# Kernel tuning notes

Hardware: AMD Instinct MI355X
Metric: run time of the kernel (lower is better)

The kernel has to match this reference:

```python
import jax, jax.numpy as jnp
import numpy as np

B, D, UD = 32, 1024, 256          # batch, chunks_dim, units_dim
ENT, NENT = 32, 64                # entity_size, n_entities
S, C = NENT * ENT, NENT + 1       # src_len (units), n_chunks
NEG_INF = float('-inf')


def setup_inputs() -> dict:
    key = jax.random.key(0)
    ks = jax.random.split(key, 9)
    source = jax.random.normal(ks[0], (B, D), jnp.float32)
    high_level_repr = jax.random.normal(ks[1], (C, B, D), jnp.float32)
    pos_embs = jax.random.normal(ks[2], (S, B, UD), jnp.float32)
    low_level_repr = jax.random.normal(ks[3], (S, B, D), jnp.float32)
    low_level_mask = jax.random.randint(ks[4], (NENT, B, ENT), 0, 2).astype(bool)
    high_level_mask = jax.random.randint(ks[5], (1, B, C), 0, 2).astype(bool)
    high_level_mask = high_level_mask.at[..., 0].set(False)  # avoid all-masked chunk softmax
    W_unit = jax.random.normal(ks[6], (UD, D), jnp.float32) / np.sqrt(D)
    W_chunk = jax.random.normal(ks[7], (D, D), jnp.float32) / np.sqrt(D)
    W_out = jax.random.normal(ks[8], (D, 2 * D), jnp.float32) / np.sqrt(2 * D)
    return {"source": source, "high_level_repr": high_level_repr, "pos_embs": pos_embs,
            "low_level_repr": low_level_repr, "low_level_mask": low_level_mask,
            "high_level_mask": high_level_mask, "W_unit": W_unit, "W_chunk": W_chunk,
            "W_out": W_out}


def reference(source, high_level_repr, pos_embs, low_level_repr,
              low_level_mask, high_level_mask, W_unit, W_chunk, W_out):
    # batch-first views (torch transposes(0,1))
    hl = jnp.swapaxes(high_level_repr, 0, 1)    # (B, C, D)
    ll = jnp.swapaxes(low_level_repr, 0, 1)     # (B, S, D)
    pe = jnp.swapaxes(pos_embs, 0, 1)           # (B, S, UD)
    ll_mask = jnp.swapaxes(low_level_mask, 0, 1)   # (B, NENT, ENT)
    hl_mask = jnp.swapaxes(high_level_mask, 0, 1)  # (B, 1, C)

    # 'general' attention scorers, tgt_len == 1
    q_u = source @ W_unit.T                      # (B, UD)
    align_units = jnp.einsum('bd,bsd->bs', q_u, pe)        # (B, S)
    q_c = source @ W_chunk.T                     # (B, D)
    align_chunks = jnp.einsum('bd,bcd->bc', q_c, hl)[:, None, :]  # (B, 1, C)

    # low-level masked softmax per entity, NaN rows -> 0
    au = align_units.reshape(B, NENT, ENT)
    au = jnp.where(ll_mask, NEG_INF, au)
    au = jax.nn.softmax(au, axis=-1)
    all_masked = jnp.all(ll_mask, axis=-1)       # (B, NENT) rows that were NaN
    au = jnp.where(all_masked[..., None], 0.0, au)
    au = au.reshape(B, 1, S)

    # high-level masked softmax, drop chunk 0, inflate to unit granularity
    ac = jnp.where(hl_mask, NEG_INF, align_chunks)
    ac = jax.nn.softmax(ac, axis=-1)[:, :, 1:]   # (B, 1, C-1)
    ac_inflated = jnp.repeat(ac, ENT, axis=-1)   # (B, 1, S)

    align_vectors = ac_inflated * au             # (B, 1, S)
    c = jnp.einsum('bts,bsd->btd', align_vectors, ll)  # (B, 1, D)
    concat = jnp.concatenate([c, source[:, None, :]], axis=-1).reshape(B, 2 * D)
    attn_h = jnp.tanh(concat @ W_out.T)          # (B, D); tanh since attn_type='general'

    return (attn_h,
            align_vectors[:, 0, :],              # (B, S)
            ac[:, 0, :],                         # (B, C-1)
            au.reshape(B, S))                    # (B, S)
```

## Files before the change

### kernel.cpp

```cpp
#include <hip/hip_runtime.h>

#define B 32
#define D 1024
#define UD 256
#define ENT 32
#define NENT 64
#define S 2048
#define C 65
#define NSLAB 8
#define SROWS 256

__device__ __forceinline__ float dot4(float4 w, const float* q) {
    return w.x * q[0] + w.y * q[1] + w.z * q[2] + w.w * q[3];
}

__global__ __launch_bounds__(256) void k_proj(const float* __restrict__ src,
                                              const float* __restrict__ Wu,
                                              const float* __restrict__ Wc,
                                              float* __restrict__ qu,
                                              float* __restrict__ qc) {
    __shared__ alignas(16) float s_src[4][D];
    __shared__ float red[4][64][4];
    int t = threadIdx.x, rg = blockIdx.x, bg = blockIdx.y;
    for (int f = t; f < 4 * (D / 4); f += 256) {
        int bb = f >> 8, i4 = f & 255;
        float4 v = *(const float4*)(src + (size_t)(bg * 4 + bb) * D + i4 * 4);
        *(float4*)(&s_src[bb][i4 * 4]) = v;
    }
    __syncthreads();
    int jl = t & 63, kq = t >> 6;
    int gj = rg * 64 + jl;
    const float* wrow = (gj < UD) ? (Wu + (size_t)gj * D) : (Wc + (size_t)(gj - UD) * D);
    const float4* wp = (const float4*)wrow + kq * 64;
    float acc[4] = {0.f, 0.f, 0.f, 0.f};
#pragma unroll 4
    for (int i = 0; i < 64; ++i) {
        float4 w = wp[i];
        int k = kq * 256 + i * 4;
#pragma unroll
        for (int bb = 0; bb < 4; ++bb) acc[bb] += dot4(w, &s_src[bb][k]);
    }
#pragma unroll
    for (int bb = 0; bb < 4; ++bb) red[kq][jl][bb] = acc[bb];
    __syncthreads();
    {
        int jl2 = t & 63, bb = t >> 6;
        float s = red[0][jl2][bb] + red[1][jl2][bb] + red[2][jl2][bb] + red[3][jl2][bb];
        int gj2 = rg * 64 + jl2, b = bg * 4 + bb;
        if (gj2 < UD) qu[b * UD + gj2] = s;
        else qc[b * D + (gj2 - UD)] = s;
    }
}

__global__ __launch_bounds__(256) void k_score(const float* __restrict__ hl,
                                               const float* __restrict__ qc,
                                               float* __restrict__ sc) {
    __shared__ float red[4];
    int c = blockIdx.x, b = blockIdx.y, t = threadIdx.x;
    const float4* hp = (const float4*)(hl + ((size_t)c * B + b) * D);
    const float4* qp = (const float4*)(qc + (size_t)b * D);
    float4 h = hp[t];
    float4 q = qp[t];
    float acc = h.x * q.x + h.y * q.y + h.z * q.z + h.w * q.w;
    for (int o = 32; o >= 1; o >>= 1) acc += __shfl_xor(acc, o);
    if ((t & 63) == 0) red[t >> 6] = acc;
    __syncthreads();
    if (t == 0) sc[b * C + c] = red[0] + red[1] + red[2] + red[3];
}

__global__ __launch_bounds__(512) void k_fused(const float* __restrict__ pe,
                                               const float* __restrict__ ll,
                                               const int* __restrict__ lmask,
                                               const int* __restrict__ hmask,
                                               const float* __restrict__ qu,
                                               const float* __restrict__ sc,
                                               float* __restrict__ pf,
                                               float* __restrict__ out_au,
                                               float* __restrict__ out_ac,
                                               float* __restrict__ out_av) {
    __shared__ alignas(16) float q[UD];
    __shared__ float s_ac[NENT];
    __shared__ float s_sc[SROWS];
    __shared__ float s_av[SROWS];
    __shared__ alignas(16) float4 s_red[256];
    int ss = blockIdx.x, b = blockIdx.y, t = threadIdx.x;

    if (t < UD) q[t] = qu[b * UD + t];

    if (t < 64) {
        bool m1 = hmask[b * C + t] != 0;
        float x1 = m1 ? -1e30f : sc[b * C + t];
        float x2 = -1e30f;
        bool m2 = true;
        if (t == 0) { m2 = hmask[b * C + 64] != 0; x2 = m2 ? -1e30f : sc[b * C + 64]; }
        float mx = fmaxf(x1, x2);
        for (int o = 32; o >= 1; o >>= 1) mx = fmaxf(mx, __shfl_xor(mx, o));
        float e1 = m1 ? 0.f : __expf(x1 - mx);
        float sm = e1 + ((t == 0 && !m2) ? __expf(x2 - mx) : 0.f);
        for (int o = 32; o >= 1; o >>= 1) sm += __shfl_xor(sm, o);
        bool mc = hmask[b * C + (t + 1)] != 0;
        float xc = mc ? 0.f : sc[b * C + (t + 1)];
        float p = mc ? 0.f : __expf(xc - mx) / sm;
        s_ac[t] = p;
        if (ss == 0) out_ac[b * NENT + t] = p;
    }
    __syncthreads();

    int rg = t >> 3, r = t & 7;
#pragma unroll
    for (int pass = 0; pass < 4; ++pass) {
        int j = pass * 64 + rg;
        int s = ss * SROWS + j;
        const float4* pp = (const float4*)(pe + ((size_t)s * B + b) * UD) + r;
        float acc = 0.f;
#pragma unroll
        for (int i = 0; i < 8; ++i) {
            float4 v = pp[i * 8];
            acc += dot4(v, &q[(r + i * 8) * 4]);
        }
        for (int o = 1; o < 8; o <<= 1) acc += __shfl_xor(acc, o);
        if (r == 0) s_sc[j] = acc;
    }
    __syncthreads();

    if (t < SROWS) {
        int j = t, e = j & 31;
        int n = ss * 8 + (j >> 5);
        bool m = lmask[((size_t)n * B + b) * ENT + e] != 0;
        float v = m ? -1e30f : s_sc[j];
        float mx = v;
        for (int o = 16; o >= 1; o >>= 1) mx = fmaxf(mx, __shfl_xor(mx, o));
        float p = m ? 0.f : __expf(v - mx);
        float sm = p;
        for (int o = 16; o >= 1; o >>= 1) sm += __shfl_xor(sm, o);
        float au = (sm > 0.f) ? p / sm : 0.f;
        float av = s_ac[n] * au;
        s_av[j] = av;
        int s = ss * SROWS + j;
        out_au[b * S + s] = au;
        out_av[b * S + s] = av;
    }
    __syncthreads();

    int half = t >> 8, tt = t & 255;
    float4 acc = {0.f, 0.f, 0.f, 0.f};
    const float4* base =
        (const float4*)(ll + ((size_t)(ss * SROWS + half * 128) * B + b) * D) + tt;
#pragma unroll 8
    for (int j = 0; j < 128; ++j) {
        float4 x = base[(size_t)j * (B * D / 4)];
        float w = s_av[half * 128 + j];
        acc.x += w * x.x;
        acc.y += w * x.y;
        acc.z += w * x.z;
        acc.w += w * x.w;
    }
    if (half == 1) s_red[tt] = acc;
    __syncthreads();
    if (half == 0) {
        float4 o = s_red[tt];
        acc.x += o.x; acc.y += o.y; acc.z += o.z; acc.w += o.w;
        *(float4*)(pf + ((size_t)ss * B + b) * D + tt * 4) = acc;
    }
}

__global__ __launch_bounds__(256) void k_out(const float* __restrict__ Wo,
                                             const float* __restrict__ src,
                                             const float* __restrict__ pf,
                                             float* __restrict__ out_h) {
    __shared__ alignas(16) float cc[4][2 * D];
    __shared__ float red[4][64][4];
    int t = threadIdx.x, jg = blockIdx.x, bg = blockIdx.y;
    for (int f = t; f < 4 * (2 * D / 4); f += 256) {
        int bb = f >> 9, part = f & 511;
        int b = bg * 4 + bb;
        float4 v;
        if (part < 256) {
            float4 a = {0.f, 0.f, 0.f, 0.f};
            const float4* pp = (const float4*)(pf + (size_t)b * D) + part;
#pragma unroll
            for (int ssi = 0; ssi < NSLAB; ++ssi) {
                float4 x = pp[(size_t)ssi * (B * D / 4)];
                a.x += x.x; a.y += x.y; a.z += x.z; a.w += x.w;
            }
            v = a;
        } else {
            v = *(const float4*)(src + (size_t)b * D + (part - 256) * 4);
        }
        *(float4*)(&cc[bb][part * 4]) = v;
    }
    __syncthreads();
    int jl = t & 63, kq = t >> 6;
    int j = jg * 64 + jl;
    const float4* wp = (const float4*)(Wo + (size_t)j * 2 * D) + kq * 128;
    float acc[4] = {0.f, 0.f, 0.f, 0.f};
#pragma unroll 4
    for (int i = 0; i < 128; ++i) {
        float4 w = wp[i];
        int k = kq * 512 + i * 4;
#pragma unroll
        for (int bb = 0; bb < 4; ++bb) acc[bb] += dot4(w, &cc[bb][k]);
    }
#pragma unroll
    for (int bb = 0; bb < 4; ++bb) red[kq][jl][bb] = acc[bb];
    __syncthreads();
    {
        int jl2 = t & 63, bb = t >> 6;
        float s = red[0][jl2][bb] + red[1][jl2][bb] + red[2][jl2][bb] + red[3][jl2][bb];
        out_h[(size_t)(bg * 4 + bb) * D + jg * 64 + jl2] = tanhf(s);
    }
}

extern "C" void kernel_launch(void* const* d_in, const int* in_sizes, int n_in,
                              void* d_out, int out_size, void* d_ws, size_t ws_size,
                              hipStream_t stream) {
    const float* src = (const float*)d_in[0];
    const float* hl = (const float*)d_in[1];
    const float* pe = (const float*)d_in[2];
    const float* ll = (const float*)d_in[3];
    const int* lmask = (const int*)d_in[4];
    const int* hmask = (const int*)d_in[5];
    const float* Wu = (const float*)d_in[6];
    const float* Wc = (const float*)d_in[7];
    const float* Wo = (const float*)d_in[8];

    float* out = (float*)d_out;
    float* out_h = out;
    float* out_av = out + B * D;
    float* out_ac = out_av + B * S;
    float* out_au = out_ac + B * NENT;

    float* ws = (float*)d_ws;
    float* qu = ws;
    float* qc = qu + B * UD;
    float* scb = qc + B * D;
    float* pf = scb + B * C;

    k_proj<<<dim3(20, 8), 256, 0, stream>>>(src, Wu, Wc, qu, qc);
    k_score<<<dim3(C, B), 256, 0, stream>>>(hl, qc, scb);
    k_fused<<<dim3(NSLAB, B), 512, 0, stream>>>(pe, ll, lmask, hmask, qu, scb,
                                                pf, out_au, out_ac, out_av);
    k_out<<<dim3(16, 8), 256, 0, stream>>>(Wo, src, pf, out_h);
}
```

Baseline: 461.8 us.

## Restructure fused attention kernel to one wavefront per entity, removing block barriers

Each 64-lane wavefront now owns one entity of 32 units. Within its wave it recomputes the chunk softmax, computes the unit scores with full-wave shuffle reductions, runs the per-entity softmax, and accumulates the weighted low-level rows with four float4 loads per lane. Partial sums are combined across the 8 waves through shared memory behind a single barrier, so the earlier staging of scores and weights in shared memory and its multiple __syncthreads are gone. The cost is redundant chunk-softmax work in every wave and more shuffle reductions per score row.

```diff
diff --git a/kernel.cpp b/kernel.cpp
--- a/kernel.cpp
+++ b/kernel.cpp
@@ -8,7 +8,6 @@
 #define S 2048
 #define C 65
 #define NSLAB 8
-#define SROWS 256
 
 __device__ __forceinline__ float dot4(float4 w, const float* q) {
     return w.x * q[0] + w.y * q[1] + w.z * q[2] + w.w * q[3];
@@ -78,89 +77,81 @@
                                                float* __restrict__ out_au,
                                                float* __restrict__ out_ac,
                                                float* __restrict__ out_av) {
-    __shared__ alignas(16) float q[UD];
-    __shared__ float s_ac[NENT];
-    __shared__ float s_sc[SROWS];
-    __shared__ float s_av[SROWS];
-    __shared__ alignas(16) float4 s_red[256];
+    __shared__ alignas(16) float4 s_part[NSLAB][256];
     int ss = blockIdx.x, b = blockIdx.y, t = threadIdx.x;
-
-    if (t < UD) q[t] = qu[b * UD + t];
-
-    if (t < 64) {
-        bool m1 = hmask[b * C + t] != 0;
-        float x1 = m1 ? -1e30f : sc[b * C + t];
-        float x2 = -1e30f;
-        bool m2 = true;
-        if (t == 0) { m2 = hmask[b * C + 64] != 0; x2 = m2 ? -1e30f : sc[b * C + 64]; }
-        float mx = fmaxf(x1, x2);
-        for (int o = 32; o >= 1; o >>= 1) mx = fmaxf(mx, __shfl_xor(mx, o));
-        float e1 = m1 ? 0.f : __expf(x1 - mx);
-        float sm = e1 + ((t == 0 && !m2) ? __expf(x2 - mx) : 0.f);
-        for (int o = 32; o >= 1; o >>= 1) sm += __shfl_xor(sm, o);
-        bool mc = hmask[b * C + (t + 1)] != 0;
-        float xc = mc ? 0.f : sc[b * C + (t + 1)];
-        float p = mc ? 0.f : __expf(xc - mx) / sm;
-        s_ac[t] = p;
-        if (ss == 0) out_ac[b * NENT + t] = p;
-    }
-    __syncthreads();
-
-    int rg = t >> 3, r = t & 7;
-#pragma unroll
-    for (int pass = 0; pass < 4; ++pass) {
-        int j = pass * 64 + rg;
-        int s = ss * SROWS + j;
-        const float4* pp = (const float4*)(pe + ((size_t)s * B + b) * UD) + r;
-        float acc = 0.f;
-#pragma unroll
-        for (int i = 0; i < 8; ++i) {
-            float4 v = pp[i * 8];
-            acc += dot4(v, &q[(r + i * 8) * 4]);
+    int w = t >> 6, l = t & 63;
+    int n = ss * NSLAB + w;
+
+    bool m1 = hmask[b * C + l] != 0;
+    float x1 = m1 ? -1e30f : sc[b * C + l];
+    bool m2 = hmask[b * C + 64] != 0;
+    float x2 = m2 ? -1e30f : sc[b * C + 64];
+    float mx = x1;
+    for (int o = 32; o >= 1; o >>= 1) mx = fmaxf(mx, __shfl_xor(mx, o));
+    mx = fmaxf(mx, x2);
+    float e1 = m1 ? 0.f : __expf(x1 - mx);
+    float sm = e1;
+    for (int o = 32; o >= 1; o >>= 1) sm += __shfl_xor(sm, o);
+    float e2 = m2 ? 0.f : __expf(x2 - mx);
+    sm += e2;
+    int c = n + 1;
+    float en = (c < 64) ? __shfl(e1, c) : e2;
+    float ac = en / sm;
+    if (l == 0) out_ac[b * NENT + n] = ac;
+
+    float4 qf = ((const float4*)(qu + (size_t)b * UD))[l];
+    int s0 = n * ENT;
+    const float4* pe4 = (const float4*)pe;
+    float score = 0.f;
+#pragma unroll 4
+    for (int j = 0; j < ENT; ++j) {
+        float4 v = pe4[((size_t)(s0 + j) * B + b) * (UD / 4) + l];
+        float p = v.x * qf.x + v.y * qf.y + v.z * qf.z + v.w * qf.w;
+        for (int o = 32; o >= 1; o >>= 1) p += __shfl_xor(p, o);
+        score = (l == j) ? p : score;
+    }
+
+    int e = l & 31;
+    bool m = lmask[((size_t)n * B + b) * ENT + e] != 0;
+    float v = m ? -1e30f : score;
+    float emx = v;
+    for (int o = 16; o >= 1; o >>= 1) emx = fmaxf(emx, __shfl_xor(emx, o));
+    float p = m ? 0.f : __expf(v - emx);
+    float esm = p;
+    for (int o = 16; o >= 1; o >>= 1) esm += __shfl_xor(esm, o);
+    float au = (esm > 0.f) ? p / esm : 0.f;
+    float av = ac * au;
+    if (l < ENT) {
+        out_au[b * S + s0 + l] = au;
+        out_av[b * S + s0 + l] = av;
+    }
+
+    float4 a0 = {0.f, 0.f, 0.f, 0.f}, a1 = a0, a2 = a0, a3 = a0;
+    const float4* ll4 = (const float4*)ll;
+#pragma unroll 4
+    for (int j = 0; j < ENT; ++j) {
+        float wv = __shfl(av, j);
+        const float4* rp = ll4 + ((size_t)(s0 + j) * B + b) * (D / 4) + l;
+        float4 x0 = rp[0], x1v = rp[64], x2v = rp[128], x3v = rp[192];
+        a0.x += wv * x0.x;  a0.y += wv * x0.y;  a0.z += wv * x0.z;  a0.w += wv * x0.w;
+        a1.x += wv * x1v.x; a1.y += wv * x1v.y; a1.z += wv * x1v.z; a1.w += wv * x1v.w;
+        a2.x += wv * x2v.x; a2.y += wv * x2v.y; a2.z += wv * x2v.z; a2.w += wv * x2v.w;
+        a3.x += wv * x3v.x; a3.y += wv * x3v.y; a3.z += wv * x3v.z; a3.w += wv * x3v.w;
+    }
+    s_part[w][l] = a0;
+    s_part[w][64 + l] = a1;
+    s_part[w][128 + l] = a2;
+    s_part[w][192 + l] = a3;
+    __syncthreads();
+
+    if (t < 256) {
+        float4 r = {0.f, 0.f, 0.f, 0.f};
+#pragma unroll
+        for (int ww = 0; ww < NSLAB; ++ww) {
+            float4 x = s_part[ww][t];
+            r.x += x.x; r.y += x.y; r.z += x.z; r.w += x.w;
         }
-        for (int o = 1; o < 8; o <<= 1) acc += __shfl_xor(acc, o);
-        if (r == 0) s_sc[j] = acc;
-    }
-    __syncthreads();
-
-    if (t < SROWS) {
-        int j = t, e = j & 31;
-        int n = ss * 8 + (j >> 5);
-        bool m = lmask[((size_t)n * B + b) * ENT + e] != 0;
-        float v = m ? -1e30f : s_sc[j];
-        float mx = v;
-        for (int o = 16; o >= 1; o >>= 1) mx = fmaxf(mx, __shfl_xor(mx, o));
-        float p = m ? 0.f : __expf(v - mx);
-        float sm = p;
-        for (int o = 16; o >= 1; o >>= 1) sm += __shfl_xor(sm, o);
-        float au = (sm > 0.f) ? p / sm : 0.f;
-        float av = s_ac[n] * au;
-        s_av[j] = av;
-        int s = ss * SROWS + j;
-        out_au[b * S + s] = au;
-        out_av[b * S + s] = av;
-    }
-    __syncthreads();
-
-    int half = t >> 8, tt = t & 255;
-    float4 acc = {0.f, 0.f, 0.f, 0.f};
-    const float4* base =
-        (const float4*)(ll + ((size_t)(ss * SROWS + half * 128) * B + b) * D) + tt;
-#pragma unroll 8
-    for (int j = 0; j < 128; ++j) {
-        float4 x = base[(size_t)j * (B * D / 4)];
-        float w = s_av[half * 128 + j];
-        acc.x += w * x.x;
-        acc.y += w * x.y;
-        acc.z += w * x.z;
-        acc.w += w * x.w;
-    }
-    if (half == 1) s_red[tt] = acc;
-    __syncthreads();
-    if (half == 0) {
-        float4 o = s_red[tt];
-        acc.x += o.x; acc.y += o.y; acc.z += o.z; acc.w += o.w;
-        *(float4*)(pf + ((size_t)ss * B + b) * D + tt * 4) = acc;
+        *(float4*)(pf + ((size_t)ss * B + b) * D + t * 4) = r;
     }
 }
 
```

Measured after the change: 459.1 us (median of 2 runs). Within noise of the previous version (-0.6%).
